# Performance work log

Hardware: AMD Instinct MI355X
Metric: run time of the kernel (lower is better)

Reference implementation:

```python
import jax, jax.numpy as jnp
import numpy as np

H = 8
SPLIT = 1
# deterministic stand-in for random.shuffle(range(8)) in the original
_PERM = np.random.RandomState(0).permutation(H)
SERIES_IDX = jnp.asarray(_PERM[SPLIT:])  # 7 heads
CROSS_IDX = jnp.asarray(_PERM[:SPLIT])   # 1 head


def setup_inputs() -> dict:
    key = jax.random.key(0)
    ks = jax.random.split(key, 5)
    B, L, E = 8, 1024, 64
    shp = (B, L, H, E)
    return {
        "queries": jax.random.normal(ks[0], shp, dtype=jnp.float32),
        "keys": jax.random.normal(ks[1], shp, dtype=jnp.float32),
        "keysT": jax.random.normal(ks[2], shp, dtype=jnp.float32),
        "values": jax.random.normal(ks[3], shp, dtype=jnp.float32),
        "valuesT": jax.random.normal(ks[4], shp, dtype=jnp.float32),
    }


def reference(queries, keys, keysT, values, valuesT):
    B, L, _, E = queries.shape
    scale = 1.0 / jnp.sqrt(jnp.asarray(E, dtype=queries.dtype))
    neg_inf = jnp.asarray(-jnp.inf, dtype=queries.dtype)

    # head split (gather along head dim)
    sq = queries[:, :, SERIES_IDX]   # [B,L,7,E]
    sk = keys[:, :, SERIES_IDX]      # [B,S,7,E]
    sv = values[:, :, SERIES_IDX]    # [B,S,7,D]
    cq = queries[:, :, CROSS_IDX]    # [B,L,1,E]
    ckT = keysT[:, :, CROSS_IDX]     # [B,C,1,E]
    cvT = valuesT[:, :, CROSS_IDX]   # [B,C,1,D]

    # causal mask: True above the diagonal -> disallowed
    causal = jnp.triu(jnp.ones((L, L), dtype=bool), k=1)  # [L,L]

    # series branch
    scores = jnp.einsum('blne,bsne->bnls', sq, sk)  # [B,7,L,S]
    scores = jnp.where(causal[None, None], neg_inf, scores * scale)
    series = jax.nn.softmax(scores, axis=-1)
    V = jnp.einsum('bhls,bshd->blhd', series, sv)   # [B,L,7,D]

    # cross branch
    cscores = jnp.einsum('blme,bcme->bmlc', cq, ckT)  # [B,1,L,C]
    cscores = jnp.where(causal[None, None], neg_inf, cscores * scale)
    crosses = jax.nn.softmax(cscores, axis=-1)
    V_cross = jnp.einsum('bhlc,bchd->blhd', crosses, cvT)  # [B,L,1,D]

    return jnp.concatenate([V, V_cross], axis=2)  # [B,L,8,D]
```

## Files before the change

kernel.cpp:

```cpp
#include <hip/hip_runtime.h>
#include <math.h>

#define Lq 1024
#define Hq 8
#define Eq 64
#define LDW 72

#define SRC_HEAD_PACKED 0x64503712u

typedef __bf16 bf16_t;
typedef __bf16 bf16x8 __attribute__((ext_vector_type(8)));
typedef __bf16 bf16x4 __attribute__((ext_vector_type(4)));
typedef float floatx4 __attribute__((ext_vector_type(4)));

__device__ __forceinline__ bf16x8 cvt8(const float4 a, const float4 b) {
    bf16x8 r;
    r[0] = (bf16_t)a.x; r[1] = (bf16_t)a.y; r[2] = (bf16_t)a.z; r[3] = (bf16_t)a.w;
    r[4] = (bf16_t)b.x; r[5] = (bf16_t)b.y; r[6] = (bf16_t)b.z; r[7] = (bf16_t)b.w;
    return r;
}

__global__ __launch_bounds__(256, 2)
void attn_mfma(const float* __restrict__ Q, const float* __restrict__ Ks,
               const float* __restrict__ KTs, const float* __restrict__ Vs,
               const float* __restrict__ VTs, float* __restrict__ out) {
    const int p    = blockIdx.x;
    const int slot = blockIdx.y;
    const int b    = blockIdx.z;
    const int h    = (SRC_HEAD_PACKED >> (slot * 4)) & 0xF;
    const float* __restrict__ Kp = (slot == 7) ? KTs : Ks;
    const float* __restrict__ Vp = (slot == 7) ? VTs : Vs;
    const int pA = p, pB = 15 - p;

    const int tid  = threadIdx.x;
    const int wv   = tid >> 6;
    const int lane = tid & 63;
    const int ln16 = lane & 15;
    const int quad = lane >> 4;

    __shared__ alignas(16) unsigned short k_lds[64][LDW];
    __shared__ alignas(16) unsigned short vt_lds[64][LDW];
    __shared__ alignas(16) unsigned short pt_lds[4][16][LDW];

    const float qs = 0.125f * 1.44269504f;
    bf16x8 qfA[2], qfB[2];
    {
        const int rA = pA * 64 + wv * 16 + ln16;
        const int rB = pB * 64 + wv * 16 + ln16;
        const float* qa = Q + (((size_t)b * Lq + rA) * Hq + h) * Eq + quad * 8;
        const float* qb = Q + (((size_t)b * Lq + rB) * Hq + h) * Eq + quad * 8;
        #pragma unroll
        for (int ec = 0; ec < 2; ++ec) {
            float4 f0 = ((const float4*)(qa + ec * 32))[0];
            float4 f1 = ((const float4*)(qa + ec * 32))[1];
            float4 g0 = ((const float4*)(qb + ec * 32))[0];
            float4 g1 = ((const float4*)(qb + ec * 32))[1];
            f0.x*=qs; f0.y*=qs; f0.z*=qs; f0.w*=qs; f1.x*=qs; f1.y*=qs; f1.z*=qs; f1.w*=qs;
            g0.x*=qs; g0.y*=qs; g0.z*=qs; g0.w*=qs; g1.x*=qs; g1.y*=qs; g1.z*=qs; g1.w*=qs;
            qfA[ec] = cvt8(f0, f1);
            qfB[ec] = cvt8(g0, g1);
        }
    }

    floatx4 OA[4], OB[4];
    #pragma unroll
    for (int i = 0; i < 4; ++i) { OA[i] = (floatx4){0,0,0,0}; OB[i] = (floatx4){0,0,0,0}; }
    float mA = -INFINITY, lA = 0.f, mB = -INFINITY, lB = 0.f;

    float4 kq[4];
    float  vq[16];
    const int kj = tid >> 2, kc = (tid & 3) * 16;
    const int vd = tid & 63, vk = (tid >> 6) * 16;

    auto load_tile = [&](int kt) {
        const float* kb = Kp + (((size_t)b * Lq + kt * 64 + kj) * Hq + h) * Eq + kc;
        kq[0] = ((const float4*)kb)[0]; kq[1] = ((const float4*)kb)[1];
        kq[2] = ((const float4*)kb)[2]; kq[3] = ((const float4*)kb)[3];
        const float* vb = Vp + (((size_t)b * Lq + kt * 64 + vk) * Hq + h) * Eq + vd;
        #pragma unroll
        for (int i = 0; i < 16; ++i) vq[i] = vb[(size_t)i * (Hq * Eq)];
    };

    auto process = [&](const bf16x8* qf, bf16x8 kf[4][2], bf16x8 vf[4][2],
                       floatx4* O, float& m, float& l, bool diag) {
        floatx4 s[4];
        #pragma unroll
        for (int nc = 0; nc < 4; ++nc) {
            floatx4 acc = (floatx4){0,0,0,0};
            acc = __builtin_amdgcn_mfma_f32_16x16x32_bf16(kf[nc][0], qf[0], acc, 0, 0, 0);
            acc = __builtin_amdgcn_mfma_f32_16x16x32_bf16(kf[nc][1], qf[1], acc, 0, 0, 0);
            s[nc] = acc;
        }
        if (diag) {
            const int rin = wv * 16 + ln16;
            #pragma unroll
            for (int nc = 0; nc < 4; ++nc)
                #pragma unroll
                for (int r = 0; r < 4; ++r)
                    if (nc * 16 + quad * 4 + r > rin) s[nc][r] = -INFINITY;
        }
        float mn = s[0][0];
        #pragma unroll
        for (int nc = 0; nc < 4; ++nc)
            #pragma unroll
            for (int r = 0; r < 4; ++r) mn = fmaxf(mn, s[nc][r]);
        mn = fmaxf(mn, __shfl_xor(mn, 16, 64));
        mn = fmaxf(mn, __shfl_xor(mn, 32, 64));
        mn = fmaxf(mn, m);
        const float alpha = __builtin_amdgcn_exp2f(m - mn);
        m = mn;
        float ps = 0.f;
        float pv[4][4];
        #pragma unroll
        for (int nc = 0; nc < 4; ++nc)
            #pragma unroll
            for (int r = 0; r < 4; ++r) { pv[nc][r] = __builtin_amdgcn_exp2f(s[nc][r] - mn); ps += pv[nc][r]; }
        ps += __shfl_xor(ps, 16, 64);
        ps += __shfl_xor(ps, 32, 64);
        l = l * alpha + ps;
        #pragma unroll
        for (int dc = 0; dc < 4; ++dc) O[dc] *= alpha;
        #pragma unroll
        for (int nc = 0; nc < 4; ++nc) {
            bf16x4 pk;
            pk[0] = (bf16_t)pv[nc][0]; pk[1] = (bf16_t)pv[nc][1];
            pk[2] = (bf16_t)pv[nc][2]; pk[3] = (bf16_t)pv[nc][3];
            *(bf16x4*)&pt_lds[wv][ln16][nc * 16 + quad * 4] = pk;
        }
        bf16x8 pf0 = *(const bf16x8*)&pt_lds[wv][ln16][quad * 8];
        bf16x8 pf1 = *(const bf16x8*)&pt_lds[wv][ln16][32 + quad * 8];
        #pragma unroll
        for (int dc = 0; dc < 4; ++dc) {
            O[dc] = __builtin_amdgcn_mfma_f32_16x16x32_bf16(vf[dc][0], pf0, O[dc], 0, 0, 0);
            O[dc] = __builtin_amdgcn_mfma_f32_16x16x32_bf16(vf[dc][1], pf1, O[dc], 0, 0, 0);
        }
    };

    load_tile(0);
    for (int kt = 0; kt <= pB; ++kt) {
        __syncthreads();
        *(bf16x8*)&k_lds[kj][kc]      = cvt8(kq[0], kq[1]);
        *(bf16x8*)&k_lds[kj][kc + 8]  = cvt8(kq[2], kq[3]);
        {
            const float4* vq4 = (const float4*)vq;
            *(bf16x8*)&vt_lds[vd][vk]     = cvt8(vq4[0], vq4[1]);
            *(bf16x8*)&vt_lds[vd][vk + 8] = cvt8(vq4[2], vq4[3]);
        }
        if (kt < pB) load_tile(kt + 1);
        __syncthreads();

        bf16x8 kf[4][2], vf[4][2];
        #pragma unroll
        for (int c = 0; c < 4; ++c) {
            kf[c][0] = *(const bf16x8*)&k_lds[c * 16 + ln16][quad * 8];
            kf[c][1] = *(const bf16x8*)&k_lds[c * 16 + ln16][32 + quad * 8];
            vf[c][0] = *(const bf16x8*)&vt_lds[c * 16 + ln16][quad * 8];
            vf[c][1] = *(const bf16x8*)&vt_lds[c * 16 + ln16][32 + quad * 8];
        }
        if (kt <= pA) process(qfA, kf, vf, OA, mA, lA, kt == pA);
        process(qfB, kf, vf, OB, mB, lB, kt == pB);
    }

    {
        const float inv = 1.0f / lA;
        const int row = pA * 64 + wv * 16 + ln16;
        float* op = out + (((size_t)b * Lq + row) * Hq + slot) * Eq + quad * 4;
        #pragma unroll
        for (int dc = 0; dc < 4; ++dc) {
            float4 o; o.x = OA[dc][0] * inv; o.y = OA[dc][1] * inv;
            o.z = OA[dc][2] * inv; o.w = OA[dc][3] * inv;
            *(float4*)(op + dc * 16) = o;
        }
    }
    {
        const float inv = 1.0f / lB;
        const int row = pB * 64 + wv * 16 + ln16;
        float* op = out + (((size_t)b * Lq + row) * Hq + slot) * Eq + quad * 4;
        #pragma unroll
        for (int dc = 0; dc < 4; ++dc) {
            float4 o; o.x = OB[dc][0] * inv; o.y = OB[dc][1] * inv;
            o.z = OB[dc][2] * inv; o.w = OB[dc][3] * inv;
            *(float4*)(op + dc * 16) = o;
        }
    }
}

extern "C" void kernel_launch(void* const* d_in, const int* in_sizes, int n_in,
                              void* d_out, int out_size, void* d_ws, size_t ws_size,
                              hipStream_t stream) {
    const float* queries = (const float*)d_in[0];
    const float* keys    = (const float*)d_in[1];
    const float* keysT   = (const float*)d_in[2];
    const float* values  = (const float*)d_in[3];
    const float* valuesT = (const float*)d_in[4];
    float* out = (float*)d_out;

    dim3 grid(8, Hq, 8);
    dim3 block(256);
    attn_mfma<<<grid, block, 0, stream>>>(queries, keys, keysT, values, valuesT, out);
}
```

Baseline: 144.1 us.

## Double-buffer K/V LDS tiles with two-ahead prefetch and one barrier per tile

```diff
diff --git a/kernel.cpp b/kernel.cpp
--- a/kernel.cpp
+++ b/kernel.cpp
@@ -38,9 +38,10 @@
     const int ln16 = lane & 15;
     const int quad = lane >> 4;
 
-    __shared__ alignas(16) unsigned short k_lds[64][LDW];
-    __shared__ alignas(16) unsigned short vt_lds[64][LDW];
-    __shared__ alignas(16) unsigned short pt_lds[4][16][LDW];
+    __shared__ alignas(16) unsigned short k_lds[2][64][LDW];
+    __shared__ alignas(16) unsigned short vt_lds[2][64][LDW];
+    __shared__ alignas(16) unsigned short ptA[4][16][LDW];
+    __shared__ alignas(16) unsigned short ptB[4][16][LDW];
 
     const float qs = 0.125f * 1.44269504f;
     bf16x8 qfA[2], qfB[2];
@@ -67,11 +68,13 @@
     for (int i = 0; i < 4; ++i) { OA[i] = (floatx4){0,0,0,0}; OB[i] = (floatx4){0,0,0,0}; }
     float mA = -INFINITY, lA = 0.f, mB = -INFINITY, lB = 0.f;
 
+    const int kj = tid >> 2;
+    const int kc = ((((tid & 3) + (tid >> 2)) & 3)) * 16;
+    const int vd = lane;
+    const int vk = (((tid >> 6) + (lane >> 4)) & 3) * 16;
+
     float4 kq[4];
     float  vq[16];
-    const int kj = tid >> 2, kc = (tid & 3) * 16;
-    const int vd = tid & 63, vk = (tid >> 6) * 16;
-
     auto load_tile = [&](int kt) {
         const float* kb = Kp + (((size_t)b * Lq + kt * 64 + kj) * Hq + h) * Eq + kc;
         kq[0] = ((const float4*)kb)[0]; kq[1] = ((const float4*)kb)[1];
@@ -80,9 +83,17 @@
         #pragma unroll
         for (int i = 0; i < 16; ++i) vq[i] = vb[(size_t)i * (Hq * Eq)];
     };
-
-    auto process = [&](const bf16x8* qf, bf16x8 kf[4][2], bf16x8 vf[4][2],
-                       floatx4* O, float& m, float& l, bool diag) {
+    auto stage = [&](int buf) {
+        *(bf16x8*)&k_lds[buf][kj][kc]     = cvt8(kq[0], kq[1]);
+        *(bf16x8*)&k_lds[buf][kj][kc + 8] = cvt8(kq[2], kq[3]);
+        const float4* vq4 = (const float4*)vq;
+        *(bf16x8*)&vt_lds[buf][vd][vk]     = cvt8(vq4[0], vq4[1]);
+        *(bf16x8*)&vt_lds[buf][vd][vk + 8] = cvt8(vq4[2], vq4[3]);
+    };
+
+    auto process = [&](const bf16x8 (&qf)[2], bf16x8 (&kf)[4][2], bf16x8 (&vf)[4][2],
+                       floatx4 (&O)[4], float& m, float& l, bool diag,
+                       unsigned short (*ptw)[LDW]) {
         floatx4 s[4];
         #pragma unroll
         for (int nc = 0; nc < 4; ++nc) {
@@ -125,10 +136,10 @@
             bf16x4 pk;
             pk[0] = (bf16_t)pv[nc][0]; pk[1] = (bf16_t)pv[nc][1];
             pk[2] = (bf16_t)pv[nc][2]; pk[3] = (bf16_t)pv[nc][3];
-            *(bf16x4*)&pt_lds[wv][ln16][nc * 16 + quad * 4] = pk;
-        }
-        bf16x8 pf0 = *(const bf16x8*)&pt_lds[wv][ln16][quad * 8];
-        bf16x8 pf1 = *(const bf16x8*)&pt_lds[wv][ln16][32 + quad * 8];
+            *(bf16x4*)&ptw[ln16][nc * 16 + quad * 4] = pk;
+        }
+        bf16x8 pf0 = *(const bf16x8*)&ptw[ln16][quad * 8];
+        bf16x8 pf1 = *(const bf16x8*)&ptw[ln16][32 + quad * 8];
         #pragma unroll
         for (int dc = 0; dc < 4; ++dc) {
             O[dc] = __builtin_amdgcn_mfma_f32_16x16x32_bf16(vf[dc][0], pf0, O[dc], 0, 0, 0);
@@ -137,28 +148,25 @@
     };
 
     load_tile(0);
+    stage(0);
+    if (pB >= 1) load_tile(1);
+    __syncthreads();
+
     for (int kt = 0; kt <= pB; ++kt) {
-        __syncthreads();
-        *(bf16x8*)&k_lds[kj][kc]      = cvt8(kq[0], kq[1]);
-        *(bf16x8*)&k_lds[kj][kc + 8]  = cvt8(kq[2], kq[3]);
-        {
-            const float4* vq4 = (const float4*)vq;
-            *(bf16x8*)&vt_lds[vd][vk]     = cvt8(vq4[0], vq4[1]);
-            *(bf16x8*)&vt_lds[vd][vk + 8] = cvt8(vq4[2], vq4[3]);
-        }
-        if (kt < pB) load_tile(kt + 1);
-        __syncthreads();
-
+        const int cur = kt & 1, nxt = cur ^ 1;
         bf16x8 kf[4][2], vf[4][2];
         #pragma unroll
         for (int c = 0; c < 4; ++c) {
-            kf[c][0] = *(const bf16x8*)&k_lds[c * 16 + ln16][quad * 8];
-            kf[c][1] = *(const bf16x8*)&k_lds[c * 16 + ln16][32 + quad * 8];
-            vf[c][0] = *(const bf16x8*)&vt_lds[c * 16 + ln16][quad * 8];
-            vf[c][1] = *(const bf16x8*)&vt_lds[c * 16 + ln16][32 + quad * 8];
-        }
-        if (kt <= pA) process(qfA, kf, vf, OA, mA, lA, kt == pA);
-        process(qfB, kf, vf, OB, mB, lB, kt == pB);
+            kf[c][0] = *(const bf16x8*)&k_lds[cur][c * 16 + ln16][quad * 8];
+            kf[c][1] = *(const bf16x8*)&k_lds[cur][c * 16 + ln16][32 + quad * 8];
+            vf[c][0] = *(const bf16x8*)&vt_lds[cur][c * 16 + ln16][quad * 8];
+            vf[c][1] = *(const bf16x8*)&vt_lds[cur][c * 16 + ln16][32 + quad * 8];
+        }
+        if (kt + 1 <= pB) stage(nxt);
+        if (kt + 2 <= pB) load_tile(kt + 2);
+        if (kt <= pA) process(qfA, kf, vf, OA, mA, lA, kt == pA, ptA[wv]);
+        process(qfB, kf, vf, OB, mB, lB, kt == pB, ptB[wv]);
+        if (kt < pB) __syncthreads();
     }
 
     {
```

New measurement: 145.7 us. Within noise of the previous version (+1.1%).

## Split key tiles across two half-blocks and merge partial softmax states

Applied to the files above, without the earlier changes.

```diff
diff --git a/kernel.cpp b/kernel.cpp
--- a/kernel.cpp
+++ b/kernel.cpp
@@ -20,7 +20,7 @@
     return r;
 }
 
-__global__ __launch_bounds__(256, 2)
+__global__ __launch_bounds__(512, 4)
 void attn_mfma(const float* __restrict__ Q, const float* __restrict__ Ks,
                const float* __restrict__ KTs, const float* __restrict__ Vs,
                const float* __restrict__ VTs, float* __restrict__ out) {
@@ -33,14 +33,21 @@
     const int pA = p, pB = 15 - p;
 
     const int tid  = threadIdx.x;
-    const int wv   = tid >> 6;
+    const int half = tid >> 8;
+    const int htid = tid & 255;
+    const int wv   = htid >> 6;
     const int lane = tid & 63;
     const int ln16 = lane & 15;
     const int quad = lane >> 4;
 
-    __shared__ alignas(16) unsigned short k_lds[64][LDW];
-    __shared__ alignas(16) unsigned short vt_lds[64][LDW];
-    __shared__ alignas(16) unsigned short pt_lds[4][16][LDW];
+    __shared__ union {
+        struct {
+            unsigned short k[2][64][LDW];
+            unsigned short vt[2][64][LDW];
+            unsigned short pt[2][4][16][LDW];
+        } s;
+        float ox[2][64][68];
+    } sm;
 
     const float qs = 0.125f * 1.44269504f;
     bf16x8 qfA[2], qfB[2];
@@ -67,11 +74,13 @@
     for (int i = 0; i < 4; ++i) { OA[i] = (floatx4){0,0,0,0}; OB[i] = (floatx4){0,0,0,0}; }
     float mA = -INFINITY, lA = 0.f, mB = -INFINITY, lB = 0.f;
 
+    const int kj = htid >> 2;
+    const int kc = ((((htid & 3) + kj) & 3)) * 16;
+    const int vd = htid & 63;
+    const int vk = (((htid >> 6) + (vd >> 4)) & 3) * 16;
+
     float4 kq[4];
     float  vq[16];
-    const int kj = tid >> 2, kc = (tid & 3) * 16;
-    const int vd = tid & 63, vk = (tid >> 6) * 16;
-
     auto load_tile = [&](int kt) {
         const float* kb = Kp + (((size_t)b * Lq + kt * 64 + kj) * Hq + h) * Eq + kc;
         kq[0] = ((const float4*)kb)[0]; kq[1] = ((const float4*)kb)[1];
@@ -80,9 +89,17 @@
         #pragma unroll
         for (int i = 0; i < 16; ++i) vq[i] = vb[(size_t)i * (Hq * Eq)];
     };
-
-    auto process = [&](const bf16x8* qf, bf16x8 kf[4][2], bf16x8 vf[4][2],
-                       floatx4* O, float& m, float& l, bool diag) {
+    auto stage = [&]() {
+        *(bf16x8*)&sm.s.k[half][kj][kc]     = cvt8(kq[0], kq[1]);
+        *(bf16x8*)&sm.s.k[half][kj][kc + 8] = cvt8(kq[2], kq[3]);
+        const float4* vq4 = (const float4*)vq;
+        *(bf16x8*)&sm.s.vt[half][vd][vk]     = cvt8(vq4[0], vq4[1]);
+        *(bf16x8*)&sm.s.vt[half][vd][vk + 8] = cvt8(vq4[2], vq4[3]);
+    };
+
+    auto process = [&](const bf16x8 (&qf)[2], bf16x8 (&kf)[4][2], bf16x8 (&vf)[4][2],
+                       floatx4 (&O)[4], float& m, float& l, bool diag) {
+        unsigned short (*ptw)[LDW] = sm.s.pt[half][wv];
         floatx4 s[4];
         #pragma unroll
         for (int nc = 0; nc < 4; ++nc) {
@@ -125,10 +142,10 @@
             bf16x4 pk;
             pk[0] = (bf16_t)pv[nc][0]; pk[1] = (bf16_t)pv[nc][1];
             pk[2] = (bf16_t)pv[nc][2]; pk[3] = (bf16_t)pv[nc][3];
-            *(bf16x4*)&pt_lds[wv][ln16][nc * 16 + quad * 4] = pk;
-        }
-        bf16x8 pf0 = *(const bf16x8*)&pt_lds[wv][ln16][quad * 8];
-        bf16x8 pf1 = *(const bf16x8*)&pt_lds[wv][ln16][32 + quad * 8];
+            *(bf16x4*)&ptw[ln16][nc * 16 + quad * 4] = pk;
+        }
+        bf16x8 pf0 = *(const bf16x8*)&ptw[ln16][quad * 8];
+        bf16x8 pf1 = *(const bf16x8*)&ptw[ln16][32 + quad * 8];
         #pragma unroll
         for (int dc = 0; dc < 4; ++dc) {
             O[dc] = __builtin_amdgcn_mfma_f32_16x16x32_bf16(vf[dc][0], pf0, O[dc], 0, 0, 0);
@@ -136,51 +153,85 @@
         }
     };
 
-    load_tile(0);
-    for (int kt = 0; kt <= pB; ++kt) {
+    load_tile(half);
+    const int nmax = pB / 2 + 1;
+    for (int it = 0; it < nmax; ++it) {
+        const int kt  = 2 * it + half;
+        const bool act = (kt <= pB);
         __syncthreads();
-        *(bf16x8*)&k_lds[kj][kc]      = cvt8(kq[0], kq[1]);
-        *(bf16x8*)&k_lds[kj][kc + 8]  = cvt8(kq[2], kq[3]);
+        if (act) {
+            stage();
+            if (kt + 2 <= pB) load_tile(kt + 2);
+        }
+        __syncthreads();
+        if (act) {
+            bf16x8 kf[4][2], vf[4][2];
+            #pragma unroll
+            for (int c = 0; c < 4; ++c) {
+                kf[c][0] = *(const bf16x8*)&sm.s.k[half][c * 16 + ln16][quad * 8];
+                kf[c][1] = *(const bf16x8*)&sm.s.k[half][c * 16 + ln16][32 + quad * 8];
+                vf[c][0] = *(const bf16x8*)&sm.s.vt[half][c * 16 + ln16][quad * 8];
+                vf[c][1] = *(const bf16x8*)&sm.s.vt[half][c * 16 + ln16][32 + quad * 8];
+            }
+            if (kt <= pA) process(qfA, kf, vf, OA, mA, lA, kt == pA);
+            process(qfB, kf, vf, OB, mB, lB, kt == pB);
+        }
+    }
+
+    __syncthreads();
+    const int row = wv * 16 + ln16;
+    if (half == 1) {
+        #pragma unroll
+        for (int dc = 0; dc < 4; ++dc) {
+            float4 oa; oa.x = OA[dc][0]; oa.y = OA[dc][1]; oa.z = OA[dc][2]; oa.w = OA[dc][3];
+            *(float4*)&sm.ox[0][row][dc * 16 + quad * 4] = oa;
+            float4 ob; ob.x = OB[dc][0]; ob.y = OB[dc][1]; ob.z = OB[dc][2]; ob.w = OB[dc][3];
+            *(float4*)&sm.ox[1][row][dc * 16 + quad * 4] = ob;
+        }
+        if (quad == 0) {
+            sm.ox[0][row][64] = mA; sm.ox[0][row][65] = lA;
+            sm.ox[1][row][64] = mB; sm.ox[1][row][65] = lB;
+        }
+    }
+    __syncthreads();
+    if (half == 0) {
         {
-            const float4* vq4 = (const float4*)vq;
-            *(bf16x8*)&vt_lds[vd][vk]     = cvt8(vq4[0], vq4[1]);
-            *(bf16x8*)&vt_lds[vd][vk + 8] = cvt8(vq4[2], vq4[3]);
-        }
-        if (kt < pB) load_tile(kt + 1);
-        __syncthreads();
-
-        bf16x8 kf[4][2], vf[4][2];
-        #pragma unroll
-        for (int c = 0; c < 4; ++c) {
-            kf[c][0] = *(const bf16x8*)&k_lds[c * 16 + ln16][quad * 8];
-            kf[c][1] = *(const bf16x8*)&k_lds[c * 16 + ln16][32 + quad * 8];
-            vf[c][0] = *(const bf16x8*)&vt_lds[c * 16 + ln16][quad * 8];
-            vf[c][1] = *(const bf16x8*)&vt_lds[c * 16 + ln16][32 + quad * 8];
-        }
-        if (kt <= pA) process(qfA, kf, vf, OA, mA, lA, kt == pA);
-        process(qfB, kf, vf, OB, mB, lB, kt == pB);
-    }
-
-    {
-        const float inv = 1.0f / lA;
-        const int row = pA * 64 + wv * 16 + ln16;
-        float* op = out + (((size_t)b * Lq + row) * Hq + slot) * Eq + quad * 4;
-        #pragma unroll
-        for (int dc = 0; dc < 4; ++dc) {
-            float4 o; o.x = OA[dc][0] * inv; o.y = OA[dc][1] * inv;
-            o.z = OA[dc][2] * inv; o.w = OA[dc][3] * inv;
-            *(float4*)(op + dc * 16) = o;
-        }
-    }
-    {
-        const float inv = 1.0f / lB;
-        const int row = pB * 64 + wv * 16 + ln16;
-        float* op = out + (((size_t)b * Lq + row) * Hq + slot) * Eq + quad * 4;
-        #pragma unroll
-        for (int dc = 0; dc < 4; ++dc) {
-            float4 o; o.x = OB[dc][0] * inv; o.y = OB[dc][1] * inv;
-            o.z = OB[dc][2] * inv; o.w = OB[dc][3] * inv;
-            *(float4*)(op + dc * 16) = o;
+            const float m1 = sm.ox[0][row][64], l1 = sm.ox[0][row][65];
+            const float mm = fmaxf(mA, m1);
+            const float w0 = __builtin_amdgcn_exp2f(mA - mm);
+            const float w1 = __builtin_amdgcn_exp2f(m1 - mm);
+            const float inv = 1.0f / (lA * w0 + l1 * w1);
+            const int grow = pA * 64 + row;
+            float* op = out + (((size_t)b * Lq + grow) * Hq + slot) * Eq + quad * 4;
+            #pragma unroll
+            for (int dc = 0; dc < 4; ++dc) {
+                float4 o1 = *(const float4*)&sm.ox[0][row][dc * 16 + quad * 4];
+                float4 o;
+                o.x = (OA[dc][0] * w0 + o1.x * w1) * inv;
+                o.y = (OA[dc][1] * w0 + o1.y * w1) * inv;
+                o.z = (OA[dc][2] * w0 + o1.z * w1) * inv;
+                o.w = (OA[dc][3] * w0 + o1.w * w1) * inv;
+                *(float4*)(op + dc * 16) = o;
+            }
+        }
+        {
+            const float m1 = sm.ox[1][row][64], l1 = sm.ox[1][row][65];
+            const float mm = fmaxf(mB, m1);
+            const float w0 = __builtin_amdgcn_exp2f(mB - mm);
+            const float w1 = __builtin_amdgcn_exp2f(m1 - mm);
+            const float inv = 1.0f / (lB * w0 + l1 * w1);
+            const int grow = pB * 64 + row;
+            float* op = out + (((size_t)b * Lq + grow) * Hq + slot) * Eq + quad * 4;
+            #pragma unroll
+            for (int dc = 0; dc < 4; ++dc) {
+                float4 o1 = *(const float4*)&sm.ox[1][row][dc * 16 + quad * 4];
+                float4 o;
+                o.x = (OB[dc][0] * w0 + o1.x * w1) * inv;
+                o.y = (OB[dc][1] * w0 + o1.y * w1) * inv;
+                o.z = (OB[dc][2] * w0 + o1.z * w1) * inv;
+                o.w = (OB[dc][3] * w0 + o1.w * w1) * inv;
+                *(float4*)(op + dc * 16) = o;
+            }
         }
     }
 }
@@ -196,6 +247,6 @@
     float* out = (float*)d_out;
 
     dim3 grid(8, Hq, 8);
-    dim3 block(256);
+    dim3 block(512);
     attn_mfma<<<grid, block, 0, stream>>>(queries, keys, keysT, values, valuesT, out);
 }
```

After: 361.8 us. 2.51x slower.
